# Kernel optimization log

Hardware: AMD Instinct MI355X
Metric: run time of the kernel (lower is better)

The kernel has to match this reference:

```python
import jax, jax.numpy as jnp
import numpy as np

WINDOW = (-100000, 100000)
BINWIDTHS = np.array([100, 200, 500, 1000, 2000, 5000], dtype=np.int64)  # S=6 scales
NBINS = (WINDOW[1] - WINDOW[0]) // BINWIDTHS + 1                        # bins per scale
BINSHIFTS = WINDOW[0] // BINWIDTHS                                       # floor div (exact here)
BINCUMSTARTS = np.concatenate([np.zeros(1, dtype=np.int64), np.cumsum(NBINS)[:-1]])
N_WEIGHTS = int(NBINS.sum())  # 3746

F, C, R, D = 100000, 2, 500, 100


def setup_inputs() -> dict:
    key = jax.random.key(0)
    k1, k2, k3, k4 = jax.random.split(key, 4)
    # coordinates span the full window, including negatives
    coordinates = jax.random.randint(k1, (F, C), 0, WINDOW[1] - WINDOW[0]) + WINDOW[0]
    region_ids = jax.random.randint(k2, (F,), 0, R)
    W = jax.random.normal(k3, (R, N_WEIGHTS, D), dtype=jnp.float32) * 0.02
    bias = jax.random.normal(k4, (R, D), dtype=jnp.float32) * 0.02
    return {"coordinates": coordinates, "region_ids": region_ids, "W": W, "bias": bias}


def reference(coordinates, region_ids, W, bias):
    bw = jnp.asarray(BINWIDTHS)          # [S]
    shifts = jnp.asarray(BINSHIFTS)      # [S]
    starts = jnp.asarray(BINCUMSTARTS)   # [S]
    coords = jnp.clip(coordinates, WINDOW[0], WINDOW[1] - 1)  # [F,C]
    c = coords[None]  # [1,F,C], broadcast vs [S,1,1]
    bin_ix = c // bw[:, None, None] - shifts[:, None, None] + starts[:, None, None]  # [S,F,C]
    alpha = (c % bw[:, None, None]).astype(jnp.float32) / bw[:, None, None].astype(jnp.float32)  # [S,F,C]
    r = region_ids[None, :, None]  # [1,F,1] broadcasts with bin_ix
    w0 = W[r, bin_ix]              # [S,F,C,D] gather
    w1 = W[r, bin_ix + 1]          # [S,F,C,D] gather
    out = (jnp.einsum('sfcd,sfc->fd', w0, 1.0 - alpha)
           + jnp.einsum('sfcd,sfc->fd', w1, alpha)
           + bias[region_ids])     # [F,D]
    return out
```

## Files before the change

kernel.cpp:

```cpp
#include <hip/hip_runtime.h>

#define F_N 100000
#define C_N 2
#define R_N 500
#define D_N 100
#define NW  3746
#define D4  25


__global__ __launch_bounds__(256) void spline_enc_kernel(
    const int*   __restrict__ coords,
    const int*   __restrict__ region_ids,
    const float* __restrict__ W,
    const float* __restrict__ bias,
    float*       __restrict__ out)
{
    const int gid = blockIdx.x * blockDim.x + threadIdx.x;
    const int f = gid / D4;
    const int j = gid % D4;
    if (f >= F_N) return;

    const int r = region_ids[f];

    int c0 = coords[2 * f];
    int c1 = coords[2 * f + 1];
    c0 = min(max(c0, -100000), 99999);
    c1 = min(max(c1, -100000), 99999);
    const unsigned u0 = (unsigned)(c0 + 100000);
    const unsigned u1 = (unsigned)(c1 + 100000);

    const float4* __restrict__ Wr =
        (const float4*)(W + (size_t)r * ((size_t)NW * D_N));
    const float4* __restrict__ br =
        (const float4*)(bias + (size_t)r * D_N);

    float4 acc = br[j];

    const unsigned bws[6]   = {100u, 200u, 500u, 1000u, 2000u, 5000u};
    const int      starts[6] = {0, 2001, 3002, 3403, 3604, 3705};

#pragma unroll
    for (int s = 0; s < 6; ++s) {
        const unsigned bw = bws[s];
        const float inv_bw = 1.0f / (float)bw;
        const int st = starts[s];
#pragma unroll
        for (int c = 0; c < 2; ++c) {
            const unsigned u = (c == 0) ? u0 : u1;
            const unsigned q = u / bw;
            const unsigned rem = u - q * bw;
            const float alpha = (float)rem * inv_bw;
            const float oma = 1.0f - alpha;
            const size_t row = (size_t)(q + (unsigned)st) * D4 + j;
            const float4 w0 = Wr[row];
            const float4 w1 = Wr[row + D4];
            acc.x = fmaf(w0.x, oma, acc.x);
            acc.y = fmaf(w0.y, oma, acc.y);
            acc.z = fmaf(w0.z, oma, acc.z);
            acc.w = fmaf(w0.w, oma, acc.w);
            acc.x = fmaf(w1.x, alpha, acc.x);
            acc.y = fmaf(w1.y, alpha, acc.y);
            acc.z = fmaf(w1.z, alpha, acc.z);
            acc.w = fmaf(w1.w, alpha, acc.w);
        }
    }

    ((float4*)out)[(size_t)f * D4 + j] = acc;
}

extern "C" void kernel_launch(void* const* d_in, const int* in_sizes, int n_in,
                              void* d_out, int out_size, void* d_ws, size_t ws_size,
                              hipStream_t stream) {
    const int*   coords     = (const int*)d_in[0];
    const int*   region_ids = (const int*)d_in[1];
    const float* W          = (const float*)d_in[2];
    const float* bias       = (const float*)d_in[3];
    float*       out        = (float*)d_out;

    const int total = F_N * D4;
    const int block = 256;
    const int grid  = (total + block - 1) / block;
    spline_enc_kernel<<<grid, block, 0, stream>>>(coords, region_ids, W, bias, out);
}
```

Measured before the change: 943.0 us.

## Sort features by region and map workgroups to XCDs for cache locality

Adds a counting-sort pipeline (histogram, scan, scatter) that groups features by region so consecutive threads gather from the same region's weight slab. The main kernel also remaps block indices so that contiguous chunks of sorted features land on the same XCD, letting each XCD's L2 hold a smaller set of region slabs. This is meant to cut L2/HBM traffic from the random gathers, at the cost of four extra small kernel launches and uncoalesced output writes through the permutation. The old kernel is kept as a fallback when the workspace is too small.

```diff
diff --git a/kernel.cpp b/kernel.cpp
--- a/kernel.cpp
+++ b/kernel.cpp
@@ -6,28 +6,74 @@
 #define D_N 100
 #define NW  3746
 #define D4  25
-
-
-__global__ __launch_bounds__(256) void spline_enc_kernel(
-    const int*   __restrict__ coords,
-    const int*   __restrict__ region_ids,
+#define TOTAL (F_N * D4)
+
+
+
+__global__ void k_init(int* __restrict__ counts) {
+    counts[threadIdx.x] = 0;
+}
+
+__global__ __launch_bounds__(256) void k_hist(
+    const int* __restrict__ region_ids, int* __restrict__ counts) {
+    const int f = blockIdx.x * 256 + threadIdx.x;
+    if (f < F_N) atomicAdd(&counts[region_ids[f]], 1);
+}
+
+__global__ void k_scan(const int* __restrict__ counts, int* __restrict__ cursor) {
+    __shared__ int s[512];
+    const int t = threadIdx.x;
+    const int v = (t < R_N) ? counts[t] : 0;
+    s[t] = v;
+    __syncthreads();
+    for (int off = 1; off < 512; off <<= 1) {
+        int x = (t >= off) ? s[t - off] : 0;
+        __syncthreads();
+        s[t] += x;
+        __syncthreads();
+    }
+    if (t < R_N) cursor[t] = s[t] - v;
+}
+
+__global__ __launch_bounds__(256) void k_scatter(
+    const int* __restrict__ coords, const int* __restrict__ region_ids,
+    int* __restrict__ cursor, int4* __restrict__ feat) {
+    const int f = blockIdx.x * 256 + threadIdx.x;
+    if (f >= F_N) return;
+    const int r = region_ids[f];
+    const int pos = atomicAdd(&cursor[r], 1);
+    int c0 = coords[2 * f];
+    int c1 = coords[2 * f + 1];
+    c0 = min(max(c0, -100000), 99999);
+    c1 = min(max(c1, -100000), 99999);
+    feat[pos] = make_int4(f, r, c0 + 100000, c1 + 100000);
+}
+
+
+__global__ __launch_bounds__(256) void spline_main_kernel(
+    const int4*  __restrict__ feat,
     const float* __restrict__ W,
     const float* __restrict__ bias,
     float*       __restrict__ out)
 {
-    const int gid = blockIdx.x * blockDim.x + threadIdx.x;
-    const int f = gid / D4;
-    const int j = gid % D4;
-    if (f >= F_N) return;
-
-    const int r = region_ids[f];
-
-    int c0 = coords[2 * f];
-    int c1 = coords[2 * f + 1];
-    c0 = min(max(c0, -100000), 99999);
-    c1 = min(max(c1, -100000), 99999);
-    const unsigned u0 = (unsigned)(c0 + 100000);
-    const unsigned u1 = (unsigned)(c1 + 100000);
+    const int nwg = (int)gridDim.x;
+    const int q8  = nwg >> 3;
+    const int r8  = nwg & 7;
+    const int xcd = (int)blockIdx.x & 7;
+    const int idx = (int)blockIdx.x >> 3;
+    const int wg  = (xcd < r8 ? xcd * (q8 + 1)
+                              : r8 * (q8 + 1) + (xcd - r8) * q8) + idx;
+
+    const int gid = wg * 256 + (int)threadIdx.x;
+    const int p = gid / D4;
+    const int j = gid - p * D4;
+    if (p >= F_N) return;
+
+    const int4 ft = feat[p];
+    const int f = ft.x;
+    const int r = ft.y;
+    const unsigned u0 = (unsigned)ft.z;
+    const unsigned u1 = (unsigned)ft.w;
 
     const float4* __restrict__ Wr =
         (const float4*)(W + (size_t)r * ((size_t)NW * D_N));
@@ -36,7 +82,7 @@
 
     float4 acc = br[j];
 
-    const unsigned bws[6]   = {100u, 200u, 500u, 1000u, 2000u, 5000u};
+    const unsigned bws[6]    = {100u, 200u, 500u, 1000u, 2000u, 5000u};
     const int      starts[6] = {0, 2001, 3002, 3403, 3604, 3705};
 
 #pragma unroll
@@ -68,6 +114,67 @@
     ((float4*)out)[(size_t)f * D4 + j] = acc;
 }
 
+
+__global__ __launch_bounds__(256) void spline_enc_kernel(
+    const int*   __restrict__ coords,
+    const int*   __restrict__ region_ids,
+    const float* __restrict__ W,
+    const float* __restrict__ bias,
+    float*       __restrict__ out)
+{
+    const int gid = blockIdx.x * blockDim.x + threadIdx.x;
+    const int f = gid / D4;
+    const int j = gid % D4;
+    if (f >= F_N) return;
+
+    const int r = region_ids[f];
+    int c0 = coords[2 * f];
+    int c1 = coords[2 * f + 1];
+    c0 = min(max(c0, -100000), 99999);
+    c1 = min(max(c1, -100000), 99999);
+    const unsigned u0 = (unsigned)(c0 + 100000);
+    const unsigned u1 = (unsigned)(c1 + 100000);
+
+    const float4* __restrict__ Wr =
+        (const float4*)(W + (size_t)r * ((size_t)NW * D_N));
+    const float4* __restrict__ br =
+        (const float4*)(bias + (size_t)r * D_N);
+
+    float4 acc = br[j];
+
+    const unsigned bws[6]    = {100u, 200u, 500u, 1000u, 2000u, 5000u};
+    const int      starts[6] = {0, 2001, 3002, 3403, 3604, 3705};
+
+#pragma unroll
+    for (int s = 0; s < 6; ++s) {
+        const unsigned bw = bws[s];
+        const float inv_bw = 1.0f / (float)bw;
+        const int st = starts[s];
+#pragma unroll
+        for (int c = 0; c < 2; ++c) {
+            const unsigned u = (c == 0) ? u0 : u1;
+            const unsigned q = u / bw;
+            const unsigned rem = u - q * bw;
+            const float alpha = (float)rem * inv_bw;
+            const float oma = 1.0f - alpha;
+            const size_t row = (size_t)(q + (unsigned)st) * D4 + j;
+            const float4 w0 = Wr[row];
+            const float4 w1 = Wr[row + D4];
+            acc.x = fmaf(w0.x, oma, acc.x);
+            acc.y = fmaf(w0.y, oma, acc.y);
+            acc.z = fmaf(w0.z, oma, acc.z);
+            acc.w = fmaf(w0.w, oma, acc.w);
+            acc.x = fmaf(w1.x, alpha, acc.x);
+            acc.y = fmaf(w1.y, alpha, acc.y);
+            acc.z = fmaf(w1.z, alpha, acc.z);
+            acc.w = fmaf(w1.w, alpha, acc.w);
+        }
+    }
+
+    ((float4*)out)[(size_t)f * D4 + j] = acc;
+}
+
+
 extern "C" void kernel_launch(void* const* d_in, const int* in_sizes, int n_in,
                               void* d_out, int out_size, void* d_ws, size_t ws_size,
                               hipStream_t stream) {
@@ -77,8 +184,25 @@
     const float* bias       = (const float*)d_in[3];
     float*       out        = (float*)d_out;
 
-    const int total = F_N * D4;
+    const size_t need = 4096 + sizeof(int4) * (size_t)F_N;
     const int block = 256;
-    const int grid  = (total + block - 1) / block;
-    spline_enc_kernel<<<grid, block, 0, stream>>>(coords, region_ids, W, bias, out);
-}
+    const int grid_main = (TOTAL + block - 1) / block;
+
+    if (d_ws == nullptr || ws_size < need) {
+        spline_enc_kernel<<<grid_main, block, 0, stream>>>(
+            coords, region_ids, W, bias, out);
+        return;
+    }
+
+    int*  counts = (int*)d_ws;
+    int*  cursor = (int*)((char*)d_ws + 2048);
+    int4* feat   = (int4*)((char*)d_ws + 4096);
+
+    const int grid_f = (F_N + block - 1) / block;
+
+    k_init<<<1, 512, 0, stream>>>(counts);
+    k_hist<<<grid_f, block, 0, stream>>>(region_ids, counts);
+    k_scan<<<1, 512, 0, stream>>>(counts, cursor);
+    k_scatter<<<grid_f, block, 0, stream>>>(coords, region_ids, cursor, feat);
+    spline_main_kernel<<<grid_main, block, 0, stream>>>(feat, W, bias, out);
+}
```

Result: slower. 970.9 us (+3.0%).
